# Optimization experiments

Hardware: AMD Instinct MI355X
Metric: run time of the kernel (lower is better)

The kernel has to match this reference:

```python
import jax, jax.numpy as jnp
import numpy as np

B, I, M, D, H = 2, 2048, 2048, 1024, 16
Dh = D // H


def setup_inputs() -> dict:
    key = jax.random.key(0)
    ks = jax.random.split(key, 7)
    s = 0.02
    return {
        "input_BxIxDi": jax.random.normal(ks[0], (B, I, D), jnp.float32),
        "memory_BxMxDi": jax.random.normal(ks[1], (B, M, D), jnp.float32),
        "bias_BxIxM": jnp.zeros((B, I, M), jnp.float32),
        "Wq": jax.random.normal(ks[2], (D, D), jnp.float32) * s,
        "Wk": jax.random.normal(ks[3], (D, D), jnp.float32) * s,
        "Wv": jax.random.normal(ks[4], (D, D), jnp.float32) * s,
        "Wo": jax.random.normal(ks[5], (D, D), jnp.float32) * s,
    }


def _split_heads(x_bid):  # [B, L, D] -> [B, H, L, Dh]
    b, l, _ = x_bid.shape
    return x_bid.reshape(b, l, H, Dh).transpose(0, 2, 1, 3)


def reference(input_BxIxDi, memory_BxMxDi, bias_BxIxM, Wq, Wk, Wv, Wo):
    q = _split_heads(input_BxIxDi @ Wq) * (Dh ** -0.5)  # [B,H,I,Dh]
    k = _split_heads(memory_BxMxDi @ Wk)                # [B,H,M,Dh]
    v = _split_heads(memory_BxMxDi @ Wv)                # [B,H,M,Dh]
    logits = jnp.einsum("bhid,bhmd->bhim", q, k) + bias_BxIxM[:, None, :, :]
    align = jax.nn.softmax(logits, axis=-1)             # [B,H,I,M]
    out = jnp.einsum("bhim,bhmd->bhid", align, v)       # [B,H,I,Dh]
    out = out.transpose(0, 2, 1, 3).reshape(out.shape[0], out.shape[2], D)
    out = out @ Wo                                      # [B,I,D]
    return out, align
```

## Files before the change

### kernel.cpp

```cpp
#include <hip/hip_runtime.h>

#define B_ 2
#define I_ 2048
#define M_ 2048
#define D_ 1024
#define H_ 16
#define Dh_ 64
#define SSTR 2052

typedef __bf16 bf16_t;
typedef __bf16 bf16x8 __attribute__((ext_vector_type(8)));
typedef __bf16 bf16x4 __attribute__((ext_vector_type(4)));
typedef float f32x4 __attribute__((ext_vector_type(4)));

__device__ __forceinline__ bf16_t f2b(float f) {
    union { float f; unsigned u; } in;
    in.f = f;
    unsigned r = (in.u + 0x7fffu + ((in.u >> 16) & 1u)) >> 16;
    union { unsigned short s; bf16_t b; } out;
    out.s = (unsigned short)r;
    return out.b;
}

__global__ void cast_f32_bf16(const float* __restrict__ src, bf16_t* __restrict__ dst, int n) {
    int idx = (blockIdx.x * blockDim.x + threadIdx.x) * 4;
    if (idx + 3 < n) {
        float4 v = *(const float4*)(src + idx);
        bf16x4 o;
        o[0] = f2b(v.x); o[1] = f2b(v.y); o[2] = f2b(v.z); o[3] = f2b(v.w);
        *(bf16x4*)(dst + idx) = o;
    }
}

__global__ void transpose_cast(const float* __restrict__ src, bf16_t* __restrict__ dst) {
    __shared__ float tile[32][33];
    int n0 = blockIdx.x * 32, k0 = blockIdx.y * 32;
    int tx = threadIdx.x, ty = threadIdx.y;
#pragma unroll
    for (int i = 0; i < 4; i++)
        tile[ty + i * 8][tx] = src[(size_t)(k0 + ty + i * 8) * D_ + n0 + tx];
    __syncthreads();
#pragma unroll
    for (int i = 0; i < 4; i++)
        dst[(size_t)(n0 + ty + i * 8) * D_ + k0 + tx] = f2b(tile[tx][ty + i * 8]);
}

template <int MODE>
__global__ __launch_bounds__(256) void gemm_nt(const bf16_t* __restrict__ A,
                                               const bf16_t* __restrict__ Bt,
                                               void* __restrict__ Cout, float scale) {
    constexpr int LDT = 40;
    __shared__ bf16_t As[128 * LDT];
    __shared__ bf16_t Bs[128 * LDT];
    int m0 = blockIdx.x * 128, n0 = blockIdx.y * 128;
    int tid = threadIdx.x;
    int wave = tid >> 6, lane = tid & 63, quad = lane >> 4, l16 = lane & 15;
    int wr = wave >> 1, wc = wave & 1;
    f32x4 acc[4][4] = {};

    for (int k0 = 0; k0 < D_; k0 += 32) {
#pragma unroll
        for (int c = tid; c < 512; c += 256) {
            int r = c >> 2, ko = (c & 3) * 8;
            *(bf16x8*)&As[r * LDT + ko] = *(const bf16x8*)&A[(size_t)(m0 + r) * D_ + k0 + ko];
            *(bf16x8*)&Bs[r * LDT + ko] = *(const bf16x8*)&Bt[(size_t)(n0 + r) * D_ + k0 + ko];
        }
        __syncthreads();
        bf16x8 af[4], bfr[4];
#pragma unroll
        for (int i = 0; i < 4; i++) af[i] = *(bf16x8*)&As[(wr * 64 + i * 16 + l16) * LDT + quad * 8];
#pragma unroll
        for (int j = 0; j < 4; j++) bfr[j] = *(bf16x8*)&Bs[(wc * 64 + j * 16 + l16) * LDT + quad * 8];
#pragma unroll
        for (int i = 0; i < 4; i++)
#pragma unroll
            for (int j = 0; j < 4; j++)
                acc[i][j] = __builtin_amdgcn_mfma_f32_16x16x32_bf16(af[i], bfr[j], acc[i][j], 0, 0, 0);
        __syncthreads();
    }

#pragma unroll
    for (int i = 0; i < 4; i++)
#pragma unroll
        for (int j = 0; j < 4; j++) {
            int n = n0 + wc * 64 + j * 16 + l16;
#pragma unroll
            for (int r = 0; r < 4; r++) {
                int m = m0 + wr * 64 + i * 16 + quad * 4 + r;
                float v = acc[i][j][r] * scale;
                if (MODE == 0) {
                    ((bf16_t*)Cout)[(size_t)m * D_ + n] = f2b(v);
                } else if (MODE == 1) {
                    int b = m >> 11, mm = m & 2047, h = n >> 6, d = n & 63;
                    ((bf16_t*)Cout)[(((size_t)(b * H_ + h) * Dh_ + d) << 11) + mm] = f2b(v);
                } else {
                    ((float*)Cout)[(size_t)m * D_ + n] = v;
                }
            }
        }
}

__global__ __launch_bounds__(1024) void attn_fused(const bf16_t* __restrict__ Q,
                                                   const bf16_t* __restrict__ K,
                                                   const bf16_t* __restrict__ Vt,
                                                   const float* __restrict__ bias,
                                                   float* __restrict__ align_out,
                                                   bf16_t* __restrict__ AO) {
    extern __shared__ float S[];
    __shared__ float rowinv[16];
    int i0 = blockIdx.x * 16, h = blockIdx.y, b = blockIdx.z;
    int tid = threadIdx.x, wave = tid >> 6, lane = tid & 63, quad = lane >> 4, l16 = lane & 15;

    size_t qrow = (size_t)(b * I_ + i0 + l16) * D_ + h * Dh_ + quad * 8;
    bf16x8 aq0 = *(const bf16x8*)&Q[qrow];
    bf16x8 aq1 = *(const bf16x8*)&Q[qrow + 32];

#pragma unroll
    for (int t = 0; t < 8; t++) {
        int m0 = wave * 128 + t * 16;
        size_t krow = (size_t)(b * M_ + m0 + l16) * D_ + h * Dh_ + quad * 8;
        bf16x8 bk0 = *(const bf16x8*)&K[krow];
        bf16x8 bk1 = *(const bf16x8*)&K[krow + 32];
        f32x4 acc = {};
        acc = __builtin_amdgcn_mfma_f32_16x16x32_bf16(aq0, bk0, acc, 0, 0, 0);
        acc = __builtin_amdgcn_mfma_f32_16x16x32_bf16(aq1, bk1, acc, 0, 0, 0);
#pragma unroll
        for (int r = 0; r < 4; r++) {
            int i = quad * 4 + r;
            float v = acc[r] + bias[((size_t)b * I_ + i0 + i) * M_ + m0 + l16];
            S[i * SSTR + m0 + l16] = v;
        }
    }
    __syncthreads();

    {
        int row = wave;
        float* srow = &S[row * SSTR];
        float mx = -1e30f;
#pragma unroll
        for (int t = 0; t < 8; t++) {
            float4 v = *(float4*)&srow[lane * 4 + t * 256];
            mx = fmaxf(mx, fmaxf(fmaxf(v.x, v.y), fmaxf(v.z, v.w)));
        }
#pragma unroll
        for (int off = 1; off < 64; off <<= 1) mx = fmaxf(mx, __shfl_xor(mx, off));
        float sum = 0.f;
#pragma unroll
        for (int t = 0; t < 8; t++) {
            float4 v = *(float4*)&srow[lane * 4 + t * 256];
            v.x = __expf(v.x - mx); v.y = __expf(v.y - mx);
            v.z = __expf(v.z - mx); v.w = __expf(v.w - mx);
            *(float4*)&srow[lane * 4 + t * 256] = v;
            sum += v.x + v.y + v.z + v.w;
        }
#pragma unroll
        for (int off = 1; off < 64; off <<= 1) sum += __shfl_xor(sum, off);
        if (lane == 0) rowinv[row] = 1.0f / sum;
    }
    __syncthreads();

    {
        float* dst = align_out + (((size_t)(b * H_ + h) * I_ + i0) << 11);
        for (int idx = tid; idx < 16 * 2048 / 4; idx += 1024) {
            int r = idx >> 9;
            int c = (idx & 511) * 4;
            float4 v = *(float4*)&S[r * SSTR + c];
            float iv = rowinv[r];
            v.x *= iv; v.y *= iv; v.z *= iv; v.w *= iv;
            *(float4*)&dst[((size_t)r << 11) + c] = v;
        }
    }

    {
        int cg = wave & 3, kg = wave >> 2;
        int n0 = cg * 16;
        f32x4 o0 = {}, o1 = {};
        const bf16_t* vrow = &Vt[((size_t)(b * H_ + h) * Dh_ + n0 + l16) << 11];
#pragma unroll
        for (int t = 0; t < 8; t++) {
            int kt = kg * 512 + t * 64;
            const float* arow = &S[l16 * SSTR + kt + quad * 8];
            bf16x8 a0, a1;
#pragma unroll
            for (int j = 0; j < 8; j++) a0[j] = f2b(arow[j]);
#pragma unroll
            for (int j = 0; j < 8; j++) a1[j] = f2b(arow[32 + j]);
            bf16x8 v0 = *(const bf16x8*)&vrow[kt + quad * 8];
            bf16x8 v1 = *(const bf16x8*)&vrow[kt + 32 + quad * 8];
            o0 = __builtin_amdgcn_mfma_f32_16x16x32_bf16(a0, v0, o0, 0, 0, 0);
            o1 = __builtin_amdgcn_mfma_f32_16x16x32_bf16(a1, v1, o1, 0, 0, 0);
        }
        __syncthreads();
        float* scr = &S[(size_t)wave * 512 + (size_t)lane * 8];
        *(f32x4*)scr = o0;
        *(f32x4*)(scr + 4) = o1;
        __syncthreads();
        if (kg == 0) {
#pragma unroll
            for (int w2 = 1; w2 < 4; w2++) {
                const float* p = &S[(size_t)(w2 * 4 + cg) * 512 + (size_t)lane * 8];
                f32x4 p0 = *(const f32x4*)p;
                f32x4 p1 = *(const f32x4*)(p + 4);
                o0 += p0;
                o1 += p1;
            }
#pragma unroll
            for (int r = 0; r < 4; r++) {
                int i = quad * 4 + r;
                float v = (o0[r] + o1[r]) * rowinv[i];
                AO[(size_t)(b * I_ + i0 + i) * D_ + h * Dh_ + n0 + l16] = f2b(v);
            }
        }
    }
}

extern "C" void kernel_launch(void* const* d_in, const int* in_sizes, int n_in,
                              void* d_out, int out_size, void* d_ws, size_t ws_size,
                              hipStream_t stream) {
    const float* input  = (const float*)d_in[0];
    const float* memory = (const float*)d_in[1];
    const float* bias   = (const float*)d_in[2];
    const float* Wq     = (const float*)d_in[3];
    const float* Wk     = (const float*)d_in[4];
    const float* Wv     = (const float*)d_in[5];
    const float* Wo     = (const float*)d_in[6];

    float* out   = (float*)d_out;
    float* align = out + (size_t)B_ * I_ * D_;

    char* ws = (char*)d_ws;
    const size_t nBID = (size_t)B_ * I_ * D_;
    const size_t nDD  = (size_t)D_ * D_;
    bf16_t* in_b  = (bf16_t*)ws; ws += nBID * 2;
    bf16_t* mem_b = (bf16_t*)ws; ws += nBID * 2;
    bf16_t* Wq_t  = (bf16_t*)ws; ws += nDD * 2;
    bf16_t* Wk_t  = (bf16_t*)ws; ws += nDD * 2;
    bf16_t* Wv_t  = (bf16_t*)ws; ws += nDD * 2;
    bf16_t* Wo_t  = (bf16_t*)ws; ws += nDD * 2;
    bf16_t* Qb    = (bf16_t*)ws; ws += nBID * 2;
    bf16_t* Kb    = (bf16_t*)ws; ws += nBID * 2;
    bf16_t* Vt    = (bf16_t*)ws; ws += nBID * 2;
    bf16_t* AO    = (bf16_t*)ws; ws += nBID * 2;

    cast_f32_bf16<<<nBID / 1024, 256, 0, stream>>>(input, in_b, (int)nBID);
    cast_f32_bf16<<<nBID / 1024, 256, 0, stream>>>(memory, mem_b, (int)nBID);
    dim3 tb(32, 8), tg(32, 32);
    transpose_cast<<<tg, tb, 0, stream>>>(Wq, Wq_t);
    transpose_cast<<<tg, tb, 0, stream>>>(Wk, Wk_t);
    transpose_cast<<<tg, tb, 0, stream>>>(Wv, Wv_t);
    transpose_cast<<<tg, tb, 0, stream>>>(Wo, Wo_t);

    dim3 gg(32, 8);
    gemm_nt<0><<<gg, 256, 0, stream>>>(in_b, Wq_t, Qb, 0.125f);
    gemm_nt<0><<<gg, 256, 0, stream>>>(mem_b, Wk_t, Kb, 1.0f);
    gemm_nt<1><<<gg, 256, 0, stream>>>(mem_b, Wv_t, Vt, 1.0f);

    attn_fused<<<dim3(I_ / 16, H_, B_), 1024, 16 * SSTR * 4, stream>>>(Qb, Kb, Vt, bias, align, AO);

    gemm_nt<2><<<gg, 256, 0, stream>>>(AO, Wo_t, out, 1.0f);
}
```

Before: 1.098 ms.

## Swizzle attention score LDS layout, stage V-transpose stores, use packed bf16 converts

The attention kernel drops the padded score row stride and uses an XOR swizzle on the column index, which lets the P·V stage read scores as float4 vectors without bank conflicts and convert them with the packed v_cvt_pk_bf16_f32 instruction instead of scalar rounding. The V projection GEMM now writes its transposed output through a shared-memory staging tile so each thread stores 8 contiguous bf16 values, replacing scattered 2-byte global writes. Together these target LDS bank conflicts, scalar conversion cost and uncoalesced global stores, at the price of extra barriers in the GEMM epilogue and inline asm that depends on the target ISA. The packed convert's rounding may differ slightly from the manual round-to-nearest-even helper.

New measurement: 1.109 ms. No clear change (+1.0%).

```diff
diff --git a/kernel.cpp b/kernel.cpp
--- a/kernel.cpp
+++ b/kernel.cpp
@@ -6,7 +6,7 @@
 #define D_ 1024
 #define H_ 16
 #define Dh_ 64
-#define SSTR 2052
+#define SWZ(r, c) ((c) ^ (((r) & 7) << 2))
 
 typedef __bf16 bf16_t;
 typedef __bf16 bf16x8 __attribute__((ext_vector_type(8)));
@@ -20,6 +20,12 @@
     union { unsigned short s; bf16_t b; } out;
     out.s = (unsigned short)r;
     return out.b;
+}
+
+__device__ __forceinline__ unsigned cvt_pk_bf16(float lo, float hi) {
+    unsigned r;
+    asm("v_cvt_pk_bf16_f32 %0, %1, %2" : "=v"(r) : "v"(lo), "v"(hi));
+    return r;
 }
 
 __global__ void cast_f32_bf16(const float* __restrict__ src, bf16_t* __restrict__ dst, int n) {
@@ -79,6 +85,38 @@
         __syncthreads();
     }
 
+    if (MODE == 1) {
+        bf16_t* Ts = As;
+#pragma unroll
+        for (int s = 0; s < 4; s++) {
+            __syncthreads();
+            if (wc == (s >> 1)) {
+#pragma unroll
+                for (int jj = 0; jj < 2; jj++) {
+                    int j = (s & 1) * 2 + jj;
+#pragma unroll
+                    for (int i = 0; i < 4; i++)
+#pragma unroll
+                        for (int r = 0; r < 4; r++)
+                            Ts[(jj * 16 + l16) * 136 + wr * 64 + i * 16 + quad * 4 + r] =
+                                f2b(acc[i][j][r] * scale);
+                }
+            }
+            __syncthreads();
+#pragma unroll
+            for (int it = 0; it < 2; it++) {
+                int task = it * 256 + tid;
+                int ns = task >> 4, ch = task & 15;
+                int n = n0 + s * 32 + ns;
+                int m = m0 + ch * 8;
+                int bb = m >> 11, mm = m & 2047, hh = n >> 6, d = n & 63;
+                *(bf16x8*)&((bf16_t*)Cout)[(((size_t)(bb * H_ + hh) * Dh_ + d) << 11) + mm] =
+                    *(bf16x8*)&Ts[ns * 136 + ch * 8];
+            }
+        }
+        return;
+    }
+
 #pragma unroll
     for (int i = 0; i < 4; i++)
 #pragma unroll
@@ -90,9 +128,6 @@
                 float v = acc[i][j][r] * scale;
                 if (MODE == 0) {
                     ((bf16_t*)Cout)[(size_t)m * D_ + n] = f2b(v);
-                } else if (MODE == 1) {
-                    int b = m >> 11, mm = m & 2047, h = n >> 6, d = n & 63;
-                    ((bf16_t*)Cout)[(((size_t)(b * H_ + h) * Dh_ + d) << 11) + mm] = f2b(v);
                 } else {
                     ((float*)Cout)[(size_t)m * D_ + n] = v;
                 }
@@ -128,18 +163,18 @@
         for (int r = 0; r < 4; r++) {
             int i = quad * 4 + r;
             float v = acc[r] + bias[((size_t)b * I_ + i0 + i) * M_ + m0 + l16];
-            S[i * SSTR + m0 + l16] = v;
+            S[i * 2048 + SWZ(i, m0 + l16)] = v;
         }
     }
     __syncthreads();
 
     {
         int row = wave;
-        float* srow = &S[row * SSTR];
+        float* srow = &S[row * 2048];
         float mx = -1e30f;
 #pragma unroll
         for (int t = 0; t < 8; t++) {
-            float4 v = *(float4*)&srow[lane * 4 + t * 256];
+            float4 v = *(float4*)&srow[SWZ(row, lane * 4 + t * 256)];
             mx = fmaxf(mx, fmaxf(fmaxf(v.x, v.y), fmaxf(v.z, v.w)));
         }
 #pragma unroll
@@ -147,10 +182,10 @@
         float sum = 0.f;
 #pragma unroll
         for (int t = 0; t < 8; t++) {
-            float4 v = *(float4*)&srow[lane * 4 + t * 256];
+            float4 v = *(float4*)&srow[SWZ(row, lane * 4 + t * 256)];
             v.x = __expf(v.x - mx); v.y = __expf(v.y - mx);
             v.z = __expf(v.z - mx); v.w = __expf(v.w - mx);
-            *(float4*)&srow[lane * 4 + t * 256] = v;
+            *(float4*)&srow[SWZ(row, lane * 4 + t * 256)] = v;
             sum += v.x + v.y + v.z + v.w;
         }
 #pragma unroll
@@ -164,7 +199,7 @@
         for (int idx = tid; idx < 16 * 2048 / 4; idx += 1024) {
             int r = idx >> 9;
             int c = (idx & 511) * 4;
-            float4 v = *(float4*)&S[r * SSTR + c];
+            float4 v = *(float4*)&S[r * 2048 + SWZ(r, c)];
             float iv = rowinv[r];
             v.x *= iv; v.y *= iv; v.z *= iv; v.w *= iv;
             *(float4*)&dst[((size_t)r << 11) + c] = v;
@@ -176,19 +211,24 @@
         int n0 = cg * 16;
         f32x4 o0 = {}, o1 = {};
         const bf16_t* vrow = &Vt[((size_t)(b * H_ + h) * Dh_ + n0 + l16) << 11];
+        const float* srow = &S[l16 * 2048];
 #pragma unroll
         for (int t = 0; t < 8; t++) {
             int kt = kg * 512 + t * 64;
-            const float* arow = &S[l16 * SSTR + kt + quad * 8];
-            bf16x8 a0, a1;
-#pragma unroll
-            for (int j = 0; j < 8; j++) a0[j] = f2b(arow[j]);
-#pragma unroll
-            for (int j = 0; j < 8; j++) a1[j] = f2b(arow[32 + j]);
+            int c0 = kt + quad * 8;
+            float4 f0 = *(const float4*)&srow[SWZ(l16, c0)];
+            float4 f1 = *(const float4*)&srow[SWZ(l16, c0 + 4)];
+            float4 f2 = *(const float4*)&srow[SWZ(l16, c0 + 32)];
+            float4 f3 = *(const float4*)&srow[SWZ(l16, c0 + 36)];
+            union { bf16x8 v; unsigned u[4]; } a0, a1;
+            a0.u[0] = cvt_pk_bf16(f0.x, f0.y); a0.u[1] = cvt_pk_bf16(f0.z, f0.w);
+            a0.u[2] = cvt_pk_bf16(f1.x, f1.y); a0.u[3] = cvt_pk_bf16(f1.z, f1.w);
+            a1.u[0] = cvt_pk_bf16(f2.x, f2.y); a1.u[1] = cvt_pk_bf16(f2.z, f2.w);
+            a1.u[2] = cvt_pk_bf16(f3.x, f3.y); a1.u[3] = cvt_pk_bf16(f3.z, f3.w);
             bf16x8 v0 = *(const bf16x8*)&vrow[kt + quad * 8];
             bf16x8 v1 = *(const bf16x8*)&vrow[kt + 32 + quad * 8];
-            o0 = __builtin_amdgcn_mfma_f32_16x16x32_bf16(a0, v0, o0, 0, 0, 0);
-            o1 = __builtin_amdgcn_mfma_f32_16x16x32_bf16(a1, v1, o1, 0, 0, 0);
+            o0 = __builtin_amdgcn_mfma_f32_16x16x32_bf16(a0.v, v0, o0, 0, 0, 0);
+            o1 = __builtin_amdgcn_mfma_f32_16x16x32_bf16(a1.v, v1, o1, 0, 0, 0);
         }
         __syncthreads();
         float* scr = &S[(size_t)wave * 512 + (size_t)lane * 8];
@@ -255,7 +295,7 @@
     gemm_nt<0><<<gg, 256, 0, stream>>>(mem_b, Wk_t, Kb, 1.0f);
     gemm_nt<1><<<gg, 256, 0, stream>>>(mem_b, Wv_t, Vt, 1.0f);
 
-    attn_fused<<<dim3(I_ / 16, H_, B_), 1024, 16 * SSTR * 4, stream>>>(Qb, Kb, Vt, bias, align, AO);
+    attn_fused<<<dim3(I_ / 16, H_, B_), 1024, 16 * 2048 * 4, stream>>>(Qb, Kb, Vt, bias, align, AO);
 
     gemm_nt<2><<<gg, 256, 0, stream>>>(AO, Wo_t, out, 1.0f);
 }
```
